# Kernel optimization log

Hardware: AMD Instinct MI355X
Metric: run time of the kernel (lower is better)

## Reference

```python
import jax, jax.numpy as jnp
import numpy as np

DT = 0.001  # integration time step (forward arg dt in the original module)


def force_fn(x):
    # Harmonic well stand-in for the user-supplied force function.
    return -x


def _nh_step(x, v, alpha, kT, mass, Q):
    """One Nose-Hoover step, exactly mirroring the recompute block in backward()."""
    ndof = x.shape[-1]
    v2 = (v * v).sum(-1)
    alpha = alpha + (DT / 4) * (v2 - ndof * kT) / Q
    v = v * jnp.exp(-alpha[..., None] * (DT / 2))
    v2 = (v * v).sum(-1)
    alpha = alpha + (DT / 4) * (v2 - ndof * kT) / Q
    v = v + (DT / 2) * force_fn(x) / mass
    x = x + DT * v
    v = v + (DT / 2) * force_fn(x) / mass
    v2 = (v * v).sum(-1)
    alpha = alpha + (DT / 4) * (v2 - ndof * kT) / Q
    v = v * jnp.exp(-alpha[..., None] * (DT / 2))
    v2 = (v * v).sum(-1)
    alpha = alpha + (DT / 4) * (v2 - ndof * kT) / Q
    return x, v, alpha


def setup_inputs() -> dict:
    key = jax.random.key(0)
    k1, k2 = jax.random.split(key)
    B, D = 4096, 64  # batch of systems, degrees of freedom per system
    return {
        "x0": jax.random.normal(k1, (B, D), jnp.float32),
        "v0": jax.random.normal(k2, (B, D), jnp.float32),
        "alpha0": jnp.zeros((B,), jnp.float32),
        "kT": jnp.ones((), jnp.float32),
        "mass": jnp.ones((), jnp.float32),
        "Q": jnp.ones((), jnp.float32),
        "n_steps": 1000,
        "store_every": 10,
    }


def reference(x0, v0, alpha0, kT, mass, Q, n_steps, store_every):
    n_chunks = n_steps // store_every  # assume divisibility (1000 / 10)

    def inner(c, _):
        x, v, a = c
        return _nh_step(x, v, a, kT, mass, Q), None

    def chunk(c, _):
        c, _ = jax.lax.scan(inner, c, None, length=store_every)
        return c, (c[0], c[1])  # snapshot (x, v) every store_every steps

    _, (xs, vs) = jax.lax.scan(chunk, (x0, v0, alpha0), None, length=n_chunks)
    traj_x = jnp.concatenate([x0[None], xs], axis=0)  # [n_steps//store_every + 1, B, D]
    traj_v = jnp.concatenate([v0[None], vs], axis=0)
    return traj_x, traj_v
```

## Files before the change

kernel.cpp:

```cpp
#include <hip/hip_runtime.h>

#define DT 0.001f

typedef float f4 __attribute__((ext_vector_type(4)));

template<int CTRL>
__device__ __forceinline__ float dpp_add(float v) {
    int r = __builtin_amdgcn_update_dpp(0, __float_as_int(v), CTRL, 0xf, 0xf, false);
    return v + __int_as_float(r);
}

__device__ __forceinline__ float reduce16(float t) {
    t = dpp_add<0x121>(t);
    t = dpp_add<0x122>(t);
    t = dpp_add<0x124>(t);
    t = dpp_add<0x128>(t);
    return t;
}

__device__ __forceinline__ float sumsq(const f4 a) {
    return (a.x * a.x + a.y * a.y) + (a.z * a.z + a.w * a.w);
}
__device__ __forceinline__ float dot4(const f4 a, const f4 b) {
    return (a.x * b.x + a.y * b.y) + (a.z * b.z + a.w * b.w);
}

template<int SE>
__device__ __forceinline__ void run(
    f4& x, f4& u, float& sv, float& alm,
    float Sxx0, float tSxv0, float Svv0,
    int n_chunks, int se_rt,
    float c, float c2, float cE, float c2E, float M2C2E,
    float A11, float A21,
    float G00, float G01, float G10, float G11, float G2P,
    float kc1, float kc2,
    float Ph1, float Ph2, float Pf1, float Pf2,
    f4* outx, f4* outv, int snap4, int fidx)
{
    const int se = (SE > 0) ? SE : se_rt;
    float m00 = 1.f, m01 = 0.f, m10 = 0.f, m11 = 1.f;
    float q0 = A11, q1 = 0.f, p0 = A21, p1 = 0.f;
    for (int ck = 1; ck <= n_chunks; ++ck) {
        #pragma unroll
        for (int i = 0; i < se - 1; ++i) {
            const float b = sv * DT;
            const float d = sv * A11;
            const float n00 = __builtin_fmaf(b, m10, q0);
            const float n01 = __builtin_fmaf(b, m11, q1);
            const float n10 = __builtin_fmaf(d, m10, p0);
            const float n11 = __builtin_fmaf(d, m11, p1);
            const float u1 = __builtin_fmaf(tSxv0, n11, Sxx0 * n10);
            const float r  = __builtin_fmaf(Svv0, n11 * n11, n10 * u1);
            const float a3 = __builtin_fmaf(c, r, alm);
            const float g0 = __builtin_fmaf(G01, r, G00);
            const float g1 = __builtin_fmaf(G11, r, G10);
            const float svn = __builtin_fmaf(a3, __builtin_fmaf(a3, G2P, g1), g0);
            const float k0m = __builtin_fmaf(c2, r, M2C2E);
            const float k1  = __builtin_fmaf(kc1, r, 1.0f);
            const float k2  = kc2 * r;
            const float a4m = __builtin_fmaf(a3, __builtin_fmaf(a3, k2, k1), k0m);
            alm = __builtin_fmaf(c * r, svn * svn, a4m);
            m00 = n00; m01 = n01; m10 = n10; m11 = n11;
            q0 = A11 * n00; q1 = A11 * n01;
            p0 = A21 * n00; p1 = A21 * n01;
            sv = svn;
        }
        {
            const float b = sv * DT;
            const float d = sv * A11;
            const float n00 = __builtin_fmaf(b, m10, q0);
            const float n01 = __builtin_fmaf(b, m11, q1);
            const float n10 = __builtin_fmaf(d, m10, p0);
            const float n11 = __builtin_fmaf(d, m11, p1);
            const float u1 = __builtin_fmaf(tSxv0, n11, Sxx0 * n10);
            const float r  = __builtin_fmaf(Svv0, n11 * n11, n10 * u1);
            const float a3 = __builtin_fmaf(c, r, alm);
            const float s2  = __builtin_fmaf(a3, __builtin_fmaf(a3, Ph2, Ph1), 1.0f);
            const float s2q = __builtin_fmaf(a3, __builtin_fmaf(a3, Pf2, Pf1), 1.0f);
            f4 xe = n00 * x + n01 * u;
            f4 ue = n10 * x + n11 * u;
            f4 vs = s2 * ue;
            __builtin_nontemporal_store(xe, &outx[(size_t)ck * snap4 + fidx]);
            __builtin_nontemporal_store(vs, &outv[(size_t)ck * snap4 + fidx]);
            const float Rxx = reduce16(sumsq(xe));
            const float Rxv = reduce16(dot4(xe, vs));
            const float Rvv = reduce16(sumsq(vs));
            const float r2  = r * s2q;
            const float aU4 = __builtin_fmaf(c, r2, a3 - cE);
            const float aU1 = __builtin_fmaf(c, Rvv, aU4 - cE);
            const float s1  = __builtin_fmaf(aU1, __builtin_fmaf(aU1, Ph2, Ph1), 1.0f);
            const float s1q = __builtin_fmaf(aU1, __builtin_fmaf(aU1, Pf2, Pf1), 1.0f);
            alm = __builtin_fmaf(c * Rvv, s1q, aU1 - c2E);
            sv = s1;
            x = xe; u = vs;
            Sxx0 = Rxx; tSxv0 = 2.0f * Rxv; Svv0 = Rvv;
            m00 = 1.f; m01 = 0.f; m10 = 0.f; m11 = 1.f;
            q0 = A11; q1 = 0.f; p0 = A21; p1 = 0.f;
        }
    }
}

__global__ __launch_bounds__(256) void nh_kernel(
    const float* __restrict__ x0, const float* __restrict__ v0,
    const float* __restrict__ alpha0,
    const float* __restrict__ kT_p, const float* __restrict__ mass_p,
    const float* __restrict__ Q_p,
    const int* __restrict__ n_steps_p, const int* __restrict__ store_every_p,
    float* __restrict__ out, int B)
{
    const int D = 64;
    const int gid = blockIdx.x * blockDim.x + threadIdx.x;
    const int sys = gid >> 4;
    const int g   = gid & 15;
    if (sys >= B) return;

    const int n_steps = *n_steps_p;
    const int se      = *store_every_p;
    const int n_chunks = n_steps / se;

    const float kt = *kT_p, m = *mass_p, q = *Q_p;
    const float c   = 0.25f * DT / q;
    const float E   = (float)D * kt;
    const float cE  = c * E;
    const float c2  = 2.0f * c;
    const float c2E = 2.0f * cE;
    const float M2C2E = -2.0f * c2E;
    const float hd  = 0.5f * DT / m;
    const float hdt = 0.5f * DT;

    const float A11 = 1.0f - hd * DT;
    const float A21 = -hd * (2.0f - hd * DT);
    const float Ph1 = -hdt, Ph2 = 0.5f * hdt * hdt;
    const float Pf1 = -DT,  Pf2 = 0.5f * DT * DT;
    const float kc1 = -c2 * DT;
    const float kc2 = 0.5f * c2 * DT * DT;
    const float G00 = 1.0f - Ph1 * c2E;
    const float G01 = Ph1 * c2;
    const float G10 = 2.0f * Ph1;
    const float G11 = Ph1 * kc1;
    const float G2P = 4.0f * Ph2;

    const int snap4 = B * 16;
    const int fidx  = sys * 16 + g;

    f4 x = ((const f4*)x0)[fidx];
    f4 v = ((const f4*)v0)[fidx];
    const float al0 = alpha0[sys];

    f4* outx = (f4*)out;
    f4* outv = ((f4*)out) + (size_t)(n_chunks + 1) * snap4;

    __builtin_nontemporal_store(x, &outx[fidx]);
    __builtin_nontemporal_store(v, &outv[fidx]);

    float Svv = reduce16(sumsq(v));
    float Sxx = reduce16(sumsq(x));
    float Sxv = reduce16(dot4(x, v));

    const float a1  = __builtin_fmaf(c, Svv, al0 - cE);
    const float s1  = __builtin_fmaf(a1, __builtin_fmaf(a1, Ph2, Ph1), 1.0f);
    const float s1q = __builtin_fmaf(a1, __builtin_fmaf(a1, Pf2, Pf1), 1.0f);
    float sv = s1;
    const float r1 = Svv * s1q;
    float alm = __builtin_fmaf(c, r1, a1 - c2E);
    f4 u = v;

    if (se == 10)
        run<10>(x, u, sv, alm, Sxx, 2.0f * Sxv, Svv, n_chunks, se,
                c, c2, cE, c2E, M2C2E, A11, A21,
                G00, G01, G10, G11, G2P, kc1, kc2,
                Ph1, Ph2, Pf1, Pf2, outx, outv, snap4, fidx);
    else
        run<0>(x, u, sv, alm, Sxx, 2.0f * Sxv, Svv, n_chunks, se,
               c, c2, cE, c2E, M2C2E, A11, A21,
               G00, G01, G10, G11, G2P, kc1, kc2,
               Ph1, Ph2, Pf1, Pf2, outx, outv, snap4, fidx);
}

extern "C" void kernel_launch(void* const* d_in, const int* in_sizes, int n_in,
                              void* d_out, int out_size, void* d_ws, size_t ws_size,
                              hipStream_t stream) {
    const float* x0     = (const float*)d_in[0];
    const float* v0     = (const float*)d_in[1];
    const float* alpha0 = (const float*)d_in[2];
    const float* kT     = (const float*)d_in[3];
    const float* mass   = (const float*)d_in[4];
    const float* Q      = (const float*)d_in[5];
    const int* n_steps  = (const int*)d_in[6];
    const int* store_ev = (const int*)d_in[7];

    const int B = in_sizes[0] / 64;
    const int threads = B * 16;
    const int block = 256;
    const int grid = (threads + block - 1) / block;

    nh_kernel<<<grid, block, 0, stream>>>(x0, v0, alpha0, kT, mass, Q,
                                          n_steps, store_ev, (float*)d_out, B);
}
```

Baseline: 256.6 us.

## Split into scalar propagator-matrix kernel and parallel trajectory-apply kernel

Because force is linear, each snapshot is expressed as a cumulative 2x2 propagator applied to the initial (x0, v0). The first kernel runs one thread per system and tracks only the scalar statistics and the accumulated matrix, writing the matrices into the output buffer as scratch. A second fully parallel kernel then reconstructs every snapshot from x0 and v0, removing the serial per-chunk vector work and reductions. The risk is numerical drift, because Sxx/Sxv/Svv are propagated algebraically instead of being recomputed. The first kernel also gets low occupancy (64 blocks of 64 threads), and the template is hardwired to store_every=10.

```diff
diff --git a/kernel.cpp b/kernel.cpp
--- a/kernel.cpp
+++ b/kernel.cpp
@@ -3,20 +3,6 @@
 #define DT 0.001f
 
 typedef float f4 __attribute__((ext_vector_type(4)));
-
-template<int CTRL>
-__device__ __forceinline__ float dpp_add(float v) {
-    int r = __builtin_amdgcn_update_dpp(0, __float_as_int(v), CTRL, 0xf, 0xf, false);
-    return v + __int_as_float(r);
-}
-
-__device__ __forceinline__ float reduce16(float t) {
-    t = dpp_add<0x121>(t);
-    t = dpp_add<0x122>(t);
-    t = dpp_add<0x124>(t);
-    t = dpp_add<0x128>(t);
-    return t;
-}
 
 __device__ __forceinline__ float sumsq(const f4 a) {
     return (a.x * a.x + a.y * a.y) + (a.z * a.z + a.w * a.w);
@@ -26,81 +12,7 @@
 }
 
 template<int SE>
-__device__ __forceinline__ void run(
-    f4& x, f4& u, float& sv, float& alm,
-    float Sxx0, float tSxv0, float Svv0,
-    int n_chunks, int se_rt,
-    float c, float c2, float cE, float c2E, float M2C2E,
-    float A11, float A21,
-    float G00, float G01, float G10, float G11, float G2P,
-    float kc1, float kc2,
-    float Ph1, float Ph2, float Pf1, float Pf2,
-    f4* outx, f4* outv, int snap4, int fidx)
-{
-    const int se = (SE > 0) ? SE : se_rt;
-    float m00 = 1.f, m01 = 0.f, m10 = 0.f, m11 = 1.f;
-    float q0 = A11, q1 = 0.f, p0 = A21, p1 = 0.f;
-    for (int ck = 1; ck <= n_chunks; ++ck) {
-        #pragma unroll
-        for (int i = 0; i < se - 1; ++i) {
-            const float b = sv * DT;
-            const float d = sv * A11;
-            const float n00 = __builtin_fmaf(b, m10, q0);
-            const float n01 = __builtin_fmaf(b, m11, q1);
-            const float n10 = __builtin_fmaf(d, m10, p0);
-            const float n11 = __builtin_fmaf(d, m11, p1);
-            const float u1 = __builtin_fmaf(tSxv0, n11, Sxx0 * n10);
-            const float r  = __builtin_fmaf(Svv0, n11 * n11, n10 * u1);
-            const float a3 = __builtin_fmaf(c, r, alm);
-            const float g0 = __builtin_fmaf(G01, r, G00);
-            const float g1 = __builtin_fmaf(G11, r, G10);
-            const float svn = __builtin_fmaf(a3, __builtin_fmaf(a3, G2P, g1), g0);
-            const float k0m = __builtin_fmaf(c2, r, M2C2E);
-            const float k1  = __builtin_fmaf(kc1, r, 1.0f);
-            const float k2  = kc2 * r;
-            const float a4m = __builtin_fmaf(a3, __builtin_fmaf(a3, k2, k1), k0m);
-            alm = __builtin_fmaf(c * r, svn * svn, a4m);
-            m00 = n00; m01 = n01; m10 = n10; m11 = n11;
-            q0 = A11 * n00; q1 = A11 * n01;
-            p0 = A21 * n00; p1 = A21 * n01;
-            sv = svn;
-        }
-        {
-            const float b = sv * DT;
-            const float d = sv * A11;
-            const float n00 = __builtin_fmaf(b, m10, q0);
-            const float n01 = __builtin_fmaf(b, m11, q1);
-            const float n10 = __builtin_fmaf(d, m10, p0);
-            const float n11 = __builtin_fmaf(d, m11, p1);
-            const float u1 = __builtin_fmaf(tSxv0, n11, Sxx0 * n10);
-            const float r  = __builtin_fmaf(Svv0, n11 * n11, n10 * u1);
-            const float a3 = __builtin_fmaf(c, r, alm);
-            const float s2  = __builtin_fmaf(a3, __builtin_fmaf(a3, Ph2, Ph1), 1.0f);
-            const float s2q = __builtin_fmaf(a3, __builtin_fmaf(a3, Pf2, Pf1), 1.0f);
-            f4 xe = n00 * x + n01 * u;
-            f4 ue = n10 * x + n11 * u;
-            f4 vs = s2 * ue;
-            __builtin_nontemporal_store(xe, &outx[(size_t)ck * snap4 + fidx]);
-            __builtin_nontemporal_store(vs, &outv[(size_t)ck * snap4 + fidx]);
-            const float Rxx = reduce16(sumsq(xe));
-            const float Rxv = reduce16(dot4(xe, vs));
-            const float Rvv = reduce16(sumsq(vs));
-            const float r2  = r * s2q;
-            const float aU4 = __builtin_fmaf(c, r2, a3 - cE);
-            const float aU1 = __builtin_fmaf(c, Rvv, aU4 - cE);
-            const float s1  = __builtin_fmaf(aU1, __builtin_fmaf(aU1, Ph2, Ph1), 1.0f);
-            const float s1q = __builtin_fmaf(aU1, __builtin_fmaf(aU1, Pf2, Pf1), 1.0f);
-            alm = __builtin_fmaf(c * Rvv, s1q, aU1 - c2E);
-            sv = s1;
-            x = xe; u = vs;
-            Sxx0 = Rxx; tSxv0 = 2.0f * Rxv; Svv0 = Rvv;
-            m00 = 1.f; m01 = 0.f; m10 = 0.f; m11 = 1.f;
-            q0 = A11; q1 = 0.f; p0 = A21; p1 = 0.f;
-        }
-    }
-}
-
-__global__ __launch_bounds__(256) void nh_kernel(
+__global__ __launch_bounds__(64) void nh_scalar(
     const float* __restrict__ x0, const float* __restrict__ v0,
     const float* __restrict__ alpha0,
     const float* __restrict__ kT_p, const float* __restrict__ mass_p,
@@ -108,16 +20,15 @@
     const int* __restrict__ n_steps_p, const int* __restrict__ store_every_p,
     float* __restrict__ out, int B)
 {
-    const int D = 64;
-    const int gid = blockIdx.x * blockDim.x + threadIdx.x;
-    const int sys = gid >> 4;
-    const int g   = gid & 15;
+    const int sys = blockIdx.x * 64 + threadIdx.x;
     if (sys >= B) return;
 
     const int n_steps = *n_steps_p;
-    const int se      = *store_every_p;
-    const int n_chunks = n_steps / se;
+    const int se_rt   = *store_every_p;
+    const int se      = (SE > 0) ? SE : se_rt;
+    const int n_chunks = n_steps / se_rt;
 
+    const int D = 64;
     const float kt = *kT_p, m = *mass_p, q = *Q_p;
     const float c   = 0.25f * DT / q;
     const float E   = (float)D * kt;
@@ -140,41 +51,121 @@
     const float G11 = Ph1 * kc1;
     const float G2P = 4.0f * Ph2;
 
-    const int snap4 = B * 16;
-    const int fidx  = sys * 16 + g;
+    const f4* xr = (const f4*)x0 + (size_t)sys * 16;
+    const f4* vr = (const f4*)v0 + (size_t)sys * 16;
+    float Sxx = 0.f, Sxv = 0.f, Svv = 0.f;
+    #pragma unroll
+    for (int j = 0; j < 16; ++j) {
+        const f4 a = xr[j], bv = vr[j];
+        Sxx += sumsq(a);
+        Svv += sumsq(bv);
+        Sxv += dot4(a, bv);
+    }
+    float tSxv = 2.0f * Sxv;
 
-    f4 x = ((const f4*)x0)[fidx];
-    f4 v = ((const f4*)v0)[fidx];
     const float al0 = alpha0[sys];
+    const float a1  = __builtin_fmaf(c, Svv, al0 - cE);
+    float sv  = __builtin_fmaf(a1, __builtin_fmaf(a1, Ph2, Ph1), 1.0f);
+    const float s1q = __builtin_fmaf(a1, __builtin_fmaf(a1, Pf2, Pf1), 1.0f);
+    const float r1 = Svv * s1q;
+    float alm = __builtin_fmaf(c, r1, a1 - c2E);
+
+    float pc00 = 1.f, pc01 = 0.f, pc10 = 0.f, pc11 = 1.f;
 
     f4* outx = (f4*)out;
-    f4* outv = ((f4*)out) + (size_t)(n_chunks + 1) * snap4;
+    const int snap4 = B * 16;
 
-    __builtin_nontemporal_store(x, &outx[fidx]);
-    __builtin_nontemporal_store(v, &outv[fidx]);
+    for (int ck = 1; ck <= n_chunks; ++ck) {
+        float m00 = 1.f, m01 = 0.f, m10 = 0.f, m11 = 1.f;
+        float q0 = A11, q1 = 0.f, p0 = A21, p1 = 0.f;
+        #pragma unroll
+        for (int i = 0; i < se - 1; ++i) {
+            const float b = sv * DT;
+            const float d = sv * A11;
+            const float n00 = __builtin_fmaf(b, m10, q0);
+            const float n01 = __builtin_fmaf(b, m11, q1);
+            const float n10 = __builtin_fmaf(d, m10, p0);
+            const float n11 = __builtin_fmaf(d, m11, p1);
+            const float u1 = __builtin_fmaf(tSxv, n11, Sxx * n10);
+            const float r  = __builtin_fmaf(Svv, n11 * n11, n10 * u1);
+            const float a3 = __builtin_fmaf(c, r, alm);
+            const float g0 = __builtin_fmaf(G01, r, G00);
+            const float g1 = __builtin_fmaf(G11, r, G10);
+            const float svn = __builtin_fmaf(a3, __builtin_fmaf(a3, G2P, g1), g0);
+            const float k0m = __builtin_fmaf(c2, r, M2C2E);
+            const float k1  = __builtin_fmaf(kc1, r, 1.0f);
+            const float k2  = kc2 * r;
+            const float a4m = __builtin_fmaf(a3, __builtin_fmaf(a3, k2, k1), k0m);
+            alm = __builtin_fmaf(c * r, svn * svn, a4m);
+            m00 = n00; m01 = n01; m10 = n10; m11 = n11;
+            q0 = A11 * n00; q1 = A11 * n01;
+            p0 = A21 * n00; p1 = A21 * n01;
+            sv = svn;
+        }
+        const float b = sv * DT;
+        const float d = sv * A11;
+        const float n00 = __builtin_fmaf(b, m10, q0);
+        const float n01 = __builtin_fmaf(b, m11, q1);
+        const float n10 = __builtin_fmaf(d, m10, p0);
+        const float n11 = __builtin_fmaf(d, m11, p1);
+        const float u1 = __builtin_fmaf(tSxv, n11, Sxx * n10);
+        const float r  = __builtin_fmaf(Svv, n11 * n11, n10 * u1);
+        const float a3 = __builtin_fmaf(c, r, alm);
+        const float s2  = __builtin_fmaf(a3, __builtin_fmaf(a3, Ph2, Ph1), 1.0f);
+        const float s2q = __builtin_fmaf(a3, __builtin_fmaf(a3, Pf2, Pf1), 1.0f);
+        const float w2 = s2 * n10;
+        const float w3 = s2 * n11;
+        const float t00 = __builtin_fmaf(n00, pc00, n01 * pc10);
+        const float t01 = __builtin_fmaf(n00, pc01, n01 * pc11);
+        const float t10 = __builtin_fmaf(w2,  pc00, w3  * pc10);
+        const float t11 = __builtin_fmaf(w2,  pc01, w3  * pc11);
+        pc00 = t00; pc01 = t01; pc10 = t10; pc11 = t11;
+        f4 P; P.x = pc00; P.y = pc01; P.z = pc10; P.w = pc11;
+        outx[(size_t)ck * snap4 + (size_t)sys * 16] = P;
+        const float SxxN = __builtin_fmaf(n00 * n00, Sxx,
+                             __builtin_fmaf(n00 * n01, tSxv, n01 * n01 * Svv));
+        const float SxvN = __builtin_fmaf(w2 * n00, Sxx,
+                             __builtin_fmaf(0.5f * __builtin_fmaf(n00, w3, n01 * w2), tSxv,
+                                            n01 * w3 * Svv));
+        const float SvvN = r * s2q;
+        const float aU4 = __builtin_fmaf(c, SvvN, a3 - cE);
+        const float aU1 = __builtin_fmaf(c, SvvN, aU4 - cE);
+        const float s1n  = __builtin_fmaf(aU1, __builtin_fmaf(aU1, Ph2, Ph1), 1.0f);
+        const float s1qn = __builtin_fmaf(aU1, __builtin_fmaf(aU1, Pf2, Pf1), 1.0f);
+        alm = __builtin_fmaf(c * SvvN, s1qn, aU1 - c2E);
+        sv = s1n;
+        Sxx = SxxN; tSxv = 2.0f * SxvN; Svv = SvvN;
+    }
+}
 
-    float Svv = reduce16(sumsq(v));
-    float Sxx = reduce16(sumsq(x));
-    float Sxv = reduce16(dot4(x, v));
+__global__ __launch_bounds__(256) void nh_apply(
+    const float* __restrict__ x0, const float* __restrict__ v0,
+    float* __restrict__ out, int B, int n_chunks)
+{
+    const int snap4 = B * 16;
+    const int bpc = B >> 4;
+    const int ck   = blockIdx.x / bpc;
+    const int rem  = blockIdx.x - ck * bpc;
+    const int fidx = rem * 256 + threadIdx.x;
 
-    const float a1  = __builtin_fmaf(c, Svv, al0 - cE);
-    const float s1  = __builtin_fmaf(a1, __builtin_fmaf(a1, Ph2, Ph1), 1.0f);
-    const float s1q = __builtin_fmaf(a1, __builtin_fmaf(a1, Pf2, Pf1), 1.0f);
-    float sv = s1;
-    const float r1 = Svv * s1q;
-    float alm = __builtin_fmaf(c, r1, a1 - c2E);
-    f4 u = v;
+    f4* outx = (f4*)out;
+    f4* outv = outx + (size_t)(n_chunks + 1) * snap4;
 
-    if (se == 10)
-        run<10>(x, u, sv, alm, Sxx, 2.0f * Sxv, Svv, n_chunks, se,
-                c, c2, cE, c2E, M2C2E, A11, A21,
-                G00, G01, G10, G11, G2P, kc1, kc2,
-                Ph1, Ph2, Pf1, Pf2, outx, outv, snap4, fidx);
-    else
-        run<0>(x, u, sv, alm, Sxx, 2.0f * Sxv, Svv, n_chunks, se,
-               c, c2, cE, c2E, M2C2E, A11, A21,
-               G00, G01, G10, G11, G2P, kc1, kc2,
-               Ph1, Ph2, Pf1, Pf2, outx, outv, snap4, fidx);
+    const f4 xv = ((const f4*)x0)[fidx];
+    const f4 vv = ((const f4*)v0)[fidx];
+
+    if (ck == 0) {
+        __builtin_nontemporal_store(xv, &outx[fidx]);
+        __builtin_nontemporal_store(vv, &outv[fidx]);
+        return;
+    }
+
+    const int sys16 = fidx & ~15;
+    const f4 P = outx[(size_t)ck * snap4 + sys16];
+    const f4 xe = P.x * xv + P.y * vv;
+    const f4 ve = P.z * xv + P.w * vv;
+    __builtin_nontemporal_store(xe, &outx[(size_t)ck * snap4 + fidx]);
+    __builtin_nontemporal_store(ve, &outv[(size_t)ck * snap4 + fidx]);
 }
 
 extern "C" void kernel_launch(void* const* d_in, const int* in_sizes, int n_in,
@@ -190,10 +181,13 @@
     const int* store_ev = (const int*)d_in[7];
 
     const int B = in_sizes[0] / 64;
-    const int threads = B * 16;
-    const int block = 256;
-    const int grid = (threads + block - 1) / block;
+    const int n_snap   = out_size / (B * 128);
+    const int n_chunks = n_snap - 1;
 
-    nh_kernel<<<grid, block, 0, stream>>>(x0, v0, alpha0, kT, mass, Q,
-                                          n_steps, store_ev, (float*)d_out, B);
+    nh_scalar<10><<<(B + 63) / 64, 64, 0, stream>>>(
+        x0, v0, alpha0, kT, mass, Q, n_steps, store_ev, (float*)d_out, B);
+
+    const int bpc = B >> 4;
+    nh_apply<<<n_snap * bpc, 256, 0, stream>>>(
+        x0, v0, (float*)d_out, B, n_chunks);
 }
```

Result: slower. 319.1 us (+24.4%).
